# Kernel tuning notes

Hardware: AMD Instinct MI355X
Metric: run time of the kernel (lower is better)

The kernel has to match this reference:

```python
import jax, jax.numpy as jnp
import numpy as np

V = 30522
D = 768
K_DELTA = 768
BOTTLENECK = 512
B = 256
M = 4096
TEMP = 0.05
LAMBDA_REC = 1.0
LAMBDA_SPARSE = 1e-4
EPS = 1e-6


def setup_inputs() -> dict:
    key = jax.random.key(0)
    ks = jax.random.split(key, 10)
    s = lambda fan_in: 1.0 / np.sqrt(fan_in)
    return {
        "ht": jax.random.normal(ks[0], (B, V), jnp.float32),
        "sr": jax.random.uniform(ks[1], (B, V), jnp.float32),
        "z_pos": jax.random.normal(ks[2], (B, D), jnp.float32),
        "z_neg": jax.random.normal(ks[3], (M, D), jnp.float32),
        "zr": jax.random.normal(ks[4], (B, D), jnp.float32),
        "W1p": jax.random.normal(ks[5], (V, BOTTLENECK), jnp.float32) * s(V),
        "b1p": jnp.zeros((BOTTLENECK,), jnp.float32),
        "W2p": jax.random.normal(ks[6], (BOTTLENECK, V), jnp.float32) * s(BOTTLENECK),
        "b2p": jnp.zeros((V,), jnp.float32),
        "W1m": jax.random.normal(ks[7], (V, BOTTLENECK), jnp.float32) * s(V),
        "b1m": jnp.zeros((BOTTLENECK,), jnp.float32),
        "W2m": jax.random.normal(ks[8], (BOTTLENECK, V), jnp.float32) * s(BOTTLENECK),
        "b2m": jnp.zeros((V,), jnp.float32),
        "Wdec": jax.random.normal(ks[9], (V, D), jnp.float32) * s(V),
    }


def safe_l2norm(x, eps=EPS):
    return x / (jnp.linalg.norm(x, axis=-1, keepdims=True) + eps)


def _delta_branch(ht, W1, b1, W2, b2):
    # bottleneck MLP -> softplus -> topk -> scatter sparsify
    h = jax.nn.gelu(ht @ W1 + b1, approximate=False)  # torch nn.GELU default = exact erf
    u = jax.nn.softplus(h @ W2 + b2)                  # [B, V]
    vals, idx = jax.lax.top_k(u, K_DELTA)             # [B, K]
    rows = jnp.arange(u.shape[0])[:, None]
    return jnp.zeros_like(u).at[rows, idx].set(vals)  # sparse delta [B, V]


def reference(ht, sr, z_pos, z_neg, zr, W1p, b1p, W2p, b2p, W1m, b1m, W2m, b2m, Wdec):
    dsp = _delta_branch(ht, W1p, b1p, W2p, b2p)
    dsm = _delta_branch(ht, W1m, b1m, W2m, b2m)
    sqp = jnp.clip(sr + dsp, 0.0, None)
    sqm = jnp.clip(dsm, 0.0, None)
    sq = sqp - sqm
    zq = safe_l2norm(sq @ Wdec)        # DenseDecoder: Linear(V->D, bias=False) + l2norm
    zq = safe_l2norm(zq)               # re-normalized in forward_train
    z_pos_n = safe_l2norm(z_pos)
    z_neg_n = safe_l2norm(z_neg)

    pos_score = jnp.sum(zq * z_pos_n, axis=-1, keepdims=True)   # [B, 1]
    neg_score = zq @ z_neg_n.T                                   # [B, M]
    logits = jnp.concatenate([pos_score, neg_score], axis=1) / TEMP
    # cross entropy with label 0 for every row
    loss_retr = jnp.mean(jax.nn.logsumexp(logits, axis=-1) - logits[:, 0])

    zhat_r = safe_l2norm(sr @ Wdec)
    zr_n = safe_l2norm(zr)
    loss_rec = jnp.mean((zhat_r - zr_n) ** 2)

    loss_sparse = jnp.mean(jnp.sum(jnp.abs(dsp), axis=-1)) + jnp.mean(jnp.sum(jnp.abs(dsm), axis=-1))

    loss = loss_retr + LAMBDA_REC * loss_rec + LAMBDA_SPARSE * loss_sparse
    return loss
```

## Files before the change

### kernel.cpp

```cpp
#include <hip/hip_runtime.h>
#include <math.h>

#define VSZ   30522
#define DIM   768
#define KDELT 768
#define BOT   512
#define BATCH 256
#define MNEG  4096
#define EPSN  1e-6f
#define TEMPC 0.05f
#define INVT  20.0f
#define TKT   1024

typedef _Float16 f16;
typedef _Float16 f16x8 __attribute__((ext_vector_type(8)));
typedef _Float16 f16x2 __attribute__((ext_vector_type(2)));
typedef float    f32x4 __attribute__((ext_vector_type(4)));

static __device__ __forceinline__ float gelu_exact(float x){
    return 0.5f * x * (1.0f + erff(x * 0.70710678118654752440f));
}
static __device__ __forceinline__ float softplus_f(float x){
    return fmaxf(x, 0.0f) + log1pf(expf(-fabsf(x)));
}
static __device__ __forceinline__ f16x2 pkh(float a, float b){
    return __builtin_bit_cast(f16x2, __builtin_amdgcn_cvt_pkrtz(a, b));
}

template<int BSRC, int NG, int EPI, int LDA, int LDB, int N, int K, int NSPLIT>
__global__ __launch_bounds__(256, 3) void gemm32t(
    const float* __restrict__ A0, const float* __restrict__ A1,
    const float* __restrict__ B0, const float* __restrict__ B1,
    float* __restrict__ C0, float* __restrict__ C1,
    const float* __restrict__ bias0, const float* __restrict__ bias1)
{
    constexpr int MN = BATCH * N;
    __shared__ f16 Al[128][40];
    __shared__ f16 Bl[128][40];
    const int t  = threadIdx.x;
    const int m0 = blockIdx.x * 128;
    const int n0 = blockIdx.y * 128;
    const int br = blockIdx.z / NSPLIT;
    const int s  = blockIdx.z % NSPLIT;
    const float* __restrict__ A = br ? A1 : A0;
    const float* __restrict__ B = br ? B1 : B0;
    float* __restrict__ C       = br ? C1 : C0;
    const float* __restrict__ bias = br ? bias1 : bias0;

    constexpr int kchunk = ((K + NSPLIT * 32 - 1) / (NSPLIT * 32)) * 32;
    const int kb = s * kchunk;
    const int ke = min(K, kb + kchunk);

    const int ar4 = t >> 2;
    const int kq  = (t & 3) * 8;
    const int bn  = t & 127;
    const int bk2 = (t >> 7) * 16;

    const int lane = t & 63, w = t >> 6;
    const int wr = (w >> 1) * 64, wc = (w & 1) * 64;
    const int fr = lane & 15, kg = (lane >> 4) * 8;

    f32x4 acc[4][4] = {};

    float4 ra[2][2];
    float  rb[16];
    float4 rb2[2][2];

    union U8 { f16x8 v; f16x2 h[4]; };

    auto loadA = [&](int k0c, int krem) {
        #pragma unroll
        for (int p = 0; p < 2; p++) {
            const float* ap = A + (size_t)(m0 + p * 64 + ar4) * LDA + k0c + kq;
            if (krem == 32) {
                ra[p][0] = *(const float4*)ap;
                ra[p][1] = *(const float4*)(ap + 4);
            } else {
                float tm[8];
                #pragma unroll
                for (int i = 0; i < 8; i++) tm[i] = (kq + i < krem) ? ap[i] : 0.f;
                ra[p][0] = make_float4(tm[0], tm[1], tm[2], tm[3]);
                ra[p][1] = make_float4(tm[4], tm[5], tm[6], tm[7]);
            }
        }
    };
    auto loadB = [&](int k0c, int krem) {
        if (BSRC == 0) {
            const bool nok = (!NG) || (n0 + bn < N);
            if (krem == 32) {
                #pragma unroll
                for (int p = 0; p < 16; p++)
                    rb[p] = nok ? B[(size_t)(k0c + bk2 + p) * LDB + n0 + bn] : 0.f;
            } else {
                #pragma unroll
                for (int p = 0; p < 16; p++) {
                    const int kk = bk2 + p;
                    rb[p] = (kk < krem && nok) ? B[(size_t)(k0c + kk) * LDB + n0 + bn] : 0.f;
                }
            }
        } else {
            #pragma unroll
            for (int p = 0; p < 2; p++) {
                const float* bp = B + (size_t)(n0 + p * 64 + ar4) * LDB + k0c + kq;
                if (krem == 32) {
                    rb2[p][0] = *(const float4*)bp;
                    rb2[p][1] = *(const float4*)(bp + 4);
                } else {
                    float tm[8];
                    #pragma unroll
                    for (int i = 0; i < 8; i++) tm[i] = (kq + i < krem) ? bp[i] : 0.f;
                    rb2[p][0] = make_float4(tm[0], tm[1], tm[2], tm[3]);
                    rb2[p][1] = make_float4(tm[4], tm[5], tm[6], tm[7]);
                }
            }
        }
    };
    auto storeA = [&]() {
        #pragma unroll
        for (int p = 0; p < 2; p++) {
            U8 u;
            u.h[0] = pkh(ra[p][0].x, ra[p][0].y);
            u.h[1] = pkh(ra[p][0].z, ra[p][0].w);
            u.h[2] = pkh(ra[p][1].x, ra[p][1].y);
            u.h[3] = pkh(ra[p][1].z, ra[p][1].w);
            *(f16x8*)&Al[p * 64 + ar4][kq] = u.v;
        }
    };
    auto storeB = [&]() {
        if (BSRC == 0) {
            U8 u0, u1;
            u0.h[0] = pkh(rb[0],  rb[1]);
            u0.h[1] = pkh(rb[2],  rb[3]);
            u0.h[2] = pkh(rb[4],  rb[5]);
            u0.h[3] = pkh(rb[6],  rb[7]);
            u1.h[0] = pkh(rb[8],  rb[9]);
            u1.h[1] = pkh(rb[10], rb[11]);
            u1.h[2] = pkh(rb[12], rb[13]);
            u1.h[3] = pkh(rb[14], rb[15]);
            *(f16x8*)&Bl[bn][bk2]     = u0.v;
            *(f16x8*)&Bl[bn][bk2 + 8] = u1.v;
        } else {
            #pragma unroll
            for (int p = 0; p < 2; p++) {
                U8 u;
                u.h[0] = pkh(rb2[p][0].x, rb2[p][0].y);
                u.h[1] = pkh(rb2[p][0].z, rb2[p][0].w);
                u.h[2] = pkh(rb2[p][1].x, rb2[p][1].y);
                u.h[3] = pkh(rb2[p][1].z, rb2[p][1].w);
                *(f16x8*)&Bl[p * 64 + ar4][kq] = u.v;
            }
        }
    };

    int k0 = kb;
    {
        const int kr = min(32, ke - k0);
        loadA(k0, kr); loadB(k0, kr);
    }
    while (k0 < ke) {
        storeA(); storeB();
        __syncthreads();
        const int k1 = k0 + 32;
        if (k1 < ke) {
            const int kr = min(32, ke - k1);
            loadA(k1, kr); loadB(k1, kr);
        }
        f16x8 af[4], bf[4];
        #pragma unroll
        for (int m = 0; m < 4; m++) af[m] = *(const f16x8*)&Al[wr + m * 16 + fr][kg];
        #pragma unroll
        for (int n = 0; n < 4; n++) bf[n] = *(const f16x8*)&Bl[wc + n * 16 + fr][kg];
        #pragma unroll
        for (int m = 0; m < 4; m++)
            #pragma unroll
            for (int n = 0; n < 4; n++)
                acc[m][n] = __builtin_amdgcn_mfma_f32_16x16x32_f16(af[m], bf[n], acc[m][n], 0, 0, 0);
        __syncthreads();
        k0 = k1;
    }

    float* Cp = (EPI == 0) ? (C + (size_t)s * MN) : C;
    #pragma unroll
    for (int m = 0; m < 4; m++) {
        #pragma unroll
        for (int n = 0; n < 4; n++) {
            #pragma unroll
            for (int j = 0; j < 4; j++) {
                const int row = m0 + wr + m * 16 + (lane >> 4) * 4 + j;
                const int col = n0 + wc + n * 16 + fr;
                if (NG && col >= N) continue;
                if (EPI == 0) Cp[(size_t)row * N + col] = acc[m][n][j];
                else          Cp[(size_t)row * N + col] = softplus_f(acc[m][n][j] + bias[col]);
            }
        }
    }
}

__global__ __launch_bounds__(256) void reduce_bias_gelu2(
    const float* __restrict__ P0, const float* __restrict__ P1,
    const float* __restrict__ bias0, const float* __restrict__ bias1,
    float* __restrict__ H0, float* __restrict__ H1,
    int MN, int N, int nsplit)
{
    const int idx = blockIdx.x * 256 + threadIdx.x;
    if (idx >= MN) return;
    const int n = idx % N;
    const float* P = blockIdx.y ? P1 : P0;
    const float* bias = blockIdx.y ? bias1 : bias0;
    float* H = blockIdx.y ? H1 : H0;
    float s = 0.f;
    for (int k = 0; k < nsplit; k++) s += P[(size_t)k * MN + idx];
    H[idx] = gelu_exact(s + bias[n]);
}

__global__ __launch_bounds__(256) void reduce_sum_parts(
    const float* __restrict__ P, float* __restrict__ Y, int MN, int nsplit)
{
    const int idx = blockIdx.x * 256 + threadIdx.x;
    if (idx >= MN) return;
    float s = 0.f;
    for (int k = 0; k < nsplit; k++) s += P[(size_t)k * MN + idx];
    Y[idx] = s;
}

__global__ __launch_bounds__(TKT) void topk_thresh2(
    const float* __restrict__ U1, const float* __restrict__ U2,
    float* __restrict__ tP, float* __restrict__ tM)
{
    __shared__ unsigned int hist[4096];
    __shared__ unsigned int scan[TKT];
    __shared__ unsigned int s_pref;
    __shared__ int s_rem;
    const int row = blockIdx.y, t = threadIdx.x;
    const float* u = (blockIdx.x ? U2 : U1) + (size_t)row * VSZ;
    float* tout = blockIdx.x ? tM : tP;

    unsigned int pref = 0;
    int remain = KDELT;

    #pragma unroll
    for (int p = 0; p < 3; p++) {
        for (int i = t; i < 4096; i += TKT) hist[i] = 0;
        __syncthreads();
        for (int j = t; j < VSZ / 2; j += TKT) {
            const float2 x = *(const float2*)(u + 2 * j);
            const unsigned int v0 = __float_as_uint(x.x);
            const unsigned int v1 = __float_as_uint(x.y);
            if (p == 0) {
                atomicAdd(&hist[v0 >> 19], 1u);
                atomicAdd(&hist[v1 >> 19], 1u);
            } else if (p == 1) {
                if ((v0 >> 19) == pref) atomicAdd(&hist[(v0 >> 7) & 0xFFFu], 1u);
                if ((v1 >> 19) == pref) atomicAdd(&hist[(v1 >> 7) & 0xFFFu], 1u);
            } else {
                if ((v0 >> 7) == pref) atomicAdd(&hist[v0 & 0x7Fu], 1u);
                if ((v1 >> 7) == pref) atomicAdd(&hist[v1 & 0x7Fu], 1u);
            }
        }
        __syncthreads();
        unsigned int loc = hist[4 * t] + hist[4 * t + 1] + hist[4 * t + 2] + hist[4 * t + 3];
        scan[t] = loc;
        __syncthreads();
        for (int o = 1; o < TKT; o <<= 1) {
            const unsigned int v = (t + o < TKT) ? scan[t + o] : 0u;
            __syncthreads();
            scan[t] += v;
            __syncthreads();
        }
        const unsigned int above = (t + 1 < TKT) ? scan[t + 1] : 0u;
        if (scan[t] >= (unsigned int)remain && above < (unsigned int)remain) {
            unsigned int cum = above;
            #pragma unroll
            for (int bi = 3; bi >= 0; bi--) {
                const int b = 4 * t + bi;
                cum += hist[b];
                if (cum >= (unsigned int)remain) {
                    s_pref = (unsigned int)b;
                    s_rem  = remain - (int)(cum - hist[b]);
                    break;
                }
            }
        }
        __syncthreads();
        if (p == 0)      pref = s_pref;
        else if (p == 1) pref = (pref << 12) | s_pref;
        else             pref = (pref << 7)  | s_pref;
        remain = s_rem;
        __syncthreads();
    }
    if (t == 0) tout[row] = __uint_as_float(pref);
}

__global__ __launch_bounds__(256) void build_sq(
    float* __restrict__ U1, const float* __restrict__ U2,
    const float* __restrict__ sr,
    const float* __restrict__ tp, const float* __restrict__ tm,
    float* __restrict__ sparse_p, float* __restrict__ sparse_m)
{
    __shared__ float red[256];
    const int row = blockIdx.x, t = threadIdx.x;
    const float thp = tp[row], thm = tm[row];
    float* u1 = U1 + (size_t)row * VSZ;
    const float* u2 = U2 + (size_t)row * VSZ;
    const float* s  = sr + (size_t)row * VSZ;
    float sp = 0.f, sm = 0.f;
    for (int j = t; j < VSZ / 2; j += 256) {
        const float2 up = *(const float2*)(u1 + 2 * j);
        const float2 um = *(const float2*)(u2 + 2 * j);
        const float2 ss = *(const float2*)(s  + 2 * j);
        const float dp0 = (up.x >= thp) ? up.x : 0.f;
        const float dp1 = (up.y >= thp) ? up.y : 0.f;
        const float dm0 = (um.x >= thm) ? um.x : 0.f;
        const float dm1 = (um.y >= thm) ? um.y : 0.f;
        sp += dp0 + dp1; sm += dm0 + dm1;
        float2 o;
        o.x = fmaxf(ss.x + dp0, 0.f) - fmaxf(dm0, 0.f);
        o.y = fmaxf(ss.y + dp1, 0.f) - fmaxf(dm1, 0.f);
        *(float2*)(u1 + 2 * j) = o;
    }
    red[t] = sp; __syncthreads();
    for (int o = 128; o > 0; o >>= 1) { if (t < o) red[t] += red[t + o]; __syncthreads(); }
    if (t == 0) sparse_p[row] = red[0];
    __syncthreads();
    red[t] = sm; __syncthreads();
    for (int o = 128; o > 0; o >>= 1) { if (t < o) red[t] += red[t + o]; __syncthreads(); }
    if (t == 0) sparse_m[row] = red[0];
}

__global__ __launch_bounds__(256) void rownorm(
    const float* __restrict__ X, float* __restrict__ Y, int dbl)
{
    __shared__ float red[256];
    const int row = blockIdx.x, t = threadIdx.x;
    const float* x = X + (size_t)row * DIM;
    float* y = Y + (size_t)row * DIM;
    float v0 = x[t], v1 = x[t + 256], v2 = x[t + 512];
    red[t] = v0 * v0 + v1 * v1 + v2 * v2; __syncthreads();
    for (int o = 128; o > 0; o >>= 1) { if (t < o) red[t] += red[t + o]; __syncthreads(); }
    const float nrm = sqrtf(red[0]) + EPSN;
    v0 /= nrm; v1 /= nrm; v2 /= nrm;
    if (dbl) {
        __syncthreads();
        red[t] = v0 * v0 + v1 * v1 + v2 * v2; __syncthreads();
        for (int o = 128; o > 0; o >>= 1) { if (t < o) red[t] += red[t + o]; __syncthreads(); }
        const float n2 = sqrtf(red[0]) + EPSN;
        v0 /= n2; v1 /= n2; v2 /= n2;
    }
    y[t] = v0; y[t + 256] = v1; y[t + 512] = v2;
}

__global__ __launch_bounds__(256) void pos_dot(
    const float* __restrict__ zq, const float* __restrict__ zp,
    float* __restrict__ posL)
{
    __shared__ float red[256];
    const int row = blockIdx.x, t = threadIdx.x;
    const float* a = zq + (size_t)row * DIM;
    const float* b = zp + (size_t)row * DIM;
    red[t] = a[t] * b[t] + a[t + 256] * b[t + 256] + a[t + 512] * b[t + 512];
    __syncthreads();
    for (int o = 128; o > 0; o >>= 1) { if (t < o) red[t] += red[t + o]; __syncthreads(); }
    if (t == 0) posL[row] = red[0] / TEMPC;
}

__global__ __launch_bounds__(256) void lse_loss(
    const float* __restrict__ negL, const float* __restrict__ posL,
    float* __restrict__ rowL)
{
    __shared__ float red[256];
    const int row = blockIdx.x, t = threadIdx.x;
    const float* nl = negL + (size_t)row * MNEG;
    const float p = posL[row];
    float lmax = (t == 0) ? p : -INFINITY;
    for (int j = t; j < MNEG; j += 256) lmax = fmaxf(lmax, nl[j] * INVT);
    red[t] = lmax; __syncthreads();
    for (int o = 128; o > 0; o >>= 1) { if (t < o) red[t] = fmaxf(red[t], red[t + o]); __syncthreads(); }
    const float mx = red[0];
    __syncthreads();
    float lsum = (t == 0) ? expf(p - mx) : 0.f;
    for (int j = t; j < MNEG; j += 256) lsum += expf(nl[j] * INVT - mx);
    red[t] = lsum; __syncthreads();
    for (int o = 128; o > 0; o >>= 1) { if (t < o) red[t] += red[t + o]; __syncthreads(); }
    if (t == 0) rowL[row] = mx + logf(red[0]) - p;
}

__global__ __launch_bounds__(256) void rec_row(
    const float* __restrict__ zhat, const float* __restrict__ zrn,
    float* __restrict__ part)
{
    __shared__ float red[256];
    const int row = blockIdx.x, t = threadIdx.x;
    const float* a = zhat + (size_t)row * DIM;
    const float* b = zrn + (size_t)row * DIM;
    const float d0 = a[t] - b[t], d1 = a[t + 256] - b[t + 256], d2 = a[t + 512] - b[t + 512];
    red[t] = d0 * d0 + d1 * d1 + d2 * d2;
    __syncthreads();
    for (int o = 128; o > 0; o >>= 1) { if (t < o) red[t] += red[t + o]; __syncthreads(); }
    if (t == 0) part[row] = red[0];
}

__global__ __launch_bounds__(256) void final_combine(
    const float* __restrict__ rowL, const float* __restrict__ recP,
    const float* __restrict__ spP, const float* __restrict__ spM,
    float* __restrict__ out)
{
    __shared__ float red[256];
    const int t = threadIdx.x;
    red[t] = rowL[t]; __syncthreads();
    for (int o = 128; o > 0; o >>= 1) { if (t < o) red[t] += red[t + o]; __syncthreads(); }
    const float retr = red[0] / 256.0f;
    __syncthreads();
    red[t] = recP[t]; __syncthreads();
    for (int o = 128; o > 0; o >>= 1) { if (t < o) red[t] += red[t + o]; __syncthreads(); }
    const float rec = red[0] / (float)(BATCH * DIM);
    __syncthreads();
    red[t] = spP[t] + spM[t]; __syncthreads();
    for (int o = 128; o > 0; o >>= 1) { if (t < o) red[t] += red[t + o]; __syncthreads(); }
    const float sparse = red[0] / 256.0f;
    if (t == 0) out[0] = retr + 1.0f * rec + 1e-4f * sparse;
}

extern "C" void kernel_launch(void* const* d_in, const int* in_sizes, int n_in,
                              void* d_out, int out_size, void* d_ws, size_t ws_size,
                              hipStream_t stream)
{
    const float* ht   = (const float*)d_in[0];
    const float* sr   = (const float*)d_in[1];
    const float* zpos = (const float*)d_in[2];
    const float* zneg = (const float*)d_in[3];
    const float* zr   = (const float*)d_in[4];
    const float* W1p  = (const float*)d_in[5];
    const float* b1p  = (const float*)d_in[6];
    const float* W2p  = (const float*)d_in[7];
    const float* b2p  = (const float*)d_in[8];
    const float* W1m  = (const float*)d_in[9];
    const float* b1m  = (const float*)d_in[10];
    const float* W2m  = (const float*)d_in[11];
    const float* b2m  = (const float*)d_in[12];
    const float* Wdec = (const float*)d_in[13];
    float* out = (float*)d_out;

    char* ws = (char*)d_ws;
    float* U1   = (float*)(ws + 0);
    float* U2   = (float*)(ws + 31254528);
    float* P    = (float*)(ws + 62509056);
    float* Hp   = (float*)(ws + 96063488);
    float* Hm   = (float*)(ws + 96587776);
    float* Y1   = (float*)(ws + 97112064);
    float* Y2   = (float*)(ws + 97898496);
    float* Zn   = (float*)(ws + 98684928);
    float* Zp   = (float*)(ws + 111267840);
    float* Zrn  = (float*)(ws + 112054272);
    float* NegL = (float*)(ws + 112840704);
    float* tP   = (float*)(ws + 117035008);
    float* tM   = tP + 256;
    float* spP  = tP + 512;
    float* spM  = tP + 768;
    float* posL = tP + 1024;
    float* rowL = tP + 1280;
    float* recP = tP + 1536;
    (void)in_sizes; (void)n_in; (void)out_size; (void)ws_size;

    const dim3 blk(256);

    gemm32t<0,0,0, VSZ, BOT, BOT, VSZ, 56><<<dim3(2,4,112), blk, 0, stream>>>(
        ht, ht, W1p, W1m, U1, U2, nullptr, nullptr);
    reduce_bias_gelu2<<<dim3(512,2), blk, 0, stream>>>(
        U1, U2, b1p, b1m, Hp, Hm, BATCH*BOT, BOT, 56);

    gemm32t<0,1,1, BOT, VSZ, VSZ, BOT, 1><<<dim3(2,239,2), blk, 0, stream>>>(
        Hp, Hm, W2p, W2m, U1, U2, b2p, b2m);

    topk_thresh2<<<dim3(2,256), dim3(TKT), 0, stream>>>(U1, U2, tP, tM);
    build_sq<<<dim3(256), blk, 0, stream>>>(U1, U2, sr, tP, tM, spP, spM);

    gemm32t<0,0,0, VSZ, DIM, DIM, VSZ, 32><<<dim3(2,6,64), blk, 0, stream>>>(
        U1, sr, Wdec, Wdec, P, U2, nullptr, nullptr);
    reduce_sum_parts<<<dim3(768), blk, 0, stream>>>(P,  Y1, BATCH*DIM, 32);
    reduce_sum_parts<<<dim3(768), blk, 0, stream>>>(U2, Y2, BATCH*DIM, 32);

    rownorm<<<dim3(256),  blk, 0, stream>>>(Y1, Y1, 1);
    rownorm<<<dim3(256),  blk, 0, stream>>>(Y2, Y2, 0);
    rownorm<<<dim3(4096), blk, 0, stream>>>(zneg, Zn, 0);
    rownorm<<<dim3(256),  blk, 0, stream>>>(zpos, Zp, 0);
    rownorm<<<dim3(256),  blk, 0, stream>>>(zr,   Zrn, 0);

    pos_dot<<<dim3(256), blk, 0, stream>>>(Y1, Zp, posL);
    gemm32t<1,0,0, DIM, DIM, MNEG, DIM, 8><<<dim3(2,32,8), blk, 0, stream>>>(
        Y1, Y1, Zn, Zn, P, P, nullptr, nullptr);
    reduce_sum_parts<<<dim3(4096), blk, 0, stream>>>(P, NegL, BATCH*MNEG, 8);
    lse_loss<<<dim3(256), blk, 0, stream>>>(NegL, posL, rowL);

    rec_row<<<dim3(256), blk, 0, stream>>>(Y2, Zrn, recP);

    final_combine<<<dim3(1), blk, 0, stream>>>(rowL, recP, spP, spM, out);
}
```

Measured before the change: 466.6 us.

## Double-buffer LDS and prefetch registers in split-K GEMM, reduce split counts

The GEMM main loop now uses two LDS buffers and two register staging sets, so global loads for tile k+2 are issued while tile k is computed, and one barrier per iteration is removed. Launch bounds drop from 3 to 2 blocks per CU because LDS and register use grow. The first GEMM's split-K drops from 56 to 32 and writes partials into the P workspace. The negatives GEMM split drops from 8 to 4, which means fewer partial sums to reduce but fewer blocks to run in parallel.

```diff
diff --git a/kernel.cpp b/kernel.cpp
--- a/kernel.cpp
+++ b/kernel.cpp
@@ -28,15 +28,17 @@
 }
 
 template<int BSRC, int NG, int EPI, int LDA, int LDB, int N, int K, int NSPLIT>
-__global__ __launch_bounds__(256, 3) void gemm32t(
+__global__ __launch_bounds__(256, 2) void gemm32t(
     const float* __restrict__ A0, const float* __restrict__ A1,
     const float* __restrict__ B0, const float* __restrict__ B1,
     float* __restrict__ C0, float* __restrict__ C1,
     const float* __restrict__ bias0, const float* __restrict__ bias1)
 {
     constexpr int MN = BATCH * N;
-    __shared__ f16 Al[128][40];
-    __shared__ f16 Bl[128][40];
+    __shared__ f16 Al0[128][40];
+    __shared__ f16 Bl0[128][40];
+    __shared__ f16 Al1[128][40];
+    __shared__ f16 Bl1[128][40];
     const int t  = threadIdx.x;
     const int m0 = blockIdx.x * 128;
     const int n0 = blockIdx.y * 128;
@@ -62,13 +64,13 @@
 
     f32x4 acc[4][4] = {};
 
-    float4 ra[2][2];
-    float  rb[16];
-    float4 rb2[2][2];
+    float4 raS0[2][2], raS1[2][2];
+    float  rbS0[16],   rbS1[16];
+    float4 rb2S0[2][2], rb2S1[2][2];
 
     union U8 { f16x8 v; f16x2 h[4]; };
 
-    auto loadA = [&](int k0c, int krem) {
+    auto loadA = [&](int k0c, int krem, float4 (&ra)[2][2]) {
         #pragma unroll
         for (int p = 0; p < 2; p++) {
             const float* ap = A + (size_t)(m0 + p * 64 + ar4) * LDA + k0c + kq;
@@ -84,7 +86,7 @@
             }
         }
     };
-    auto loadB = [&](int k0c, int krem) {
+    auto loadB = [&](int k0c, int krem, float (&rb)[16], float4 (&rb2)[2][2]) {
         if (BSRC == 0) {
             const bool nok = (!NG) || (n0 + bn < N);
             if (krem == 32) {
@@ -115,7 +117,7 @@
             }
         }
     };
-    auto storeA = [&]() {
+    auto storeA = [&](float4 (&ra)[2][2], f16 (&Al)[128][40]) {
         #pragma unroll
         for (int p = 0; p < 2; p++) {
             U8 u;
@@ -126,7 +128,7 @@
             *(f16x8*)&Al[p * 64 + ar4][kq] = u.v;
         }
     };
-    auto storeB = [&]() {
+    auto storeB = [&](float (&rb)[16], float4 (&rb2)[2][2], f16 (&Bl)[128][40]) {
         if (BSRC == 0) {
             U8 u0, u1;
             u0.h[0] = pkh(rb[0],  rb[1]);
@@ -151,20 +153,7 @@
             }
         }
     };
-
-    int k0 = kb;
-    {
-        const int kr = min(32, ke - k0);
-        loadA(k0, kr); loadB(k0, kr);
-    }
-    while (k0 < ke) {
-        storeA(); storeB();
-        __syncthreads();
-        const int k1 = k0 + 32;
-        if (k1 < ke) {
-            const int kr = min(32, ke - k1);
-            loadA(k1, kr); loadB(k1, kr);
-        }
+    auto compute = [&](f16 (&Al)[128][40], f16 (&Bl)[128][40]) {
         f16x8 af[4], bf[4];
         #pragma unroll
         for (int m = 0; m < 4; m++) af[m] = *(const f16x8*)&Al[wr + m * 16 + fr][kg];
@@ -175,8 +164,43 @@
             #pragma unroll
             for (int n = 0; n < 4; n++)
                 acc[m][n] = __builtin_amdgcn_mfma_f32_16x16x32_f16(af[m], bf[n], acc[m][n], 0, 0, 0);
-        __syncthreads();
-        k0 = k1;
+    };
+
+    int k_next = kb;
+    {
+        const int kr = min(32, ke - k_next);
+        loadA(k_next, kr, raS0); loadB(k_next, kr, rbS0, rb2S0);
+        k_next += 32;
+    }
+    if (k_next < ke) {
+        const int kr = min(32, ke - k_next);
+        loadA(k_next, kr, raS1); loadB(k_next, kr, rbS1, rb2S1);
+        k_next += 32;
+    }
+
+    int k_comp = kb;
+    while (true) {
+        storeA(raS0, Al0); storeB(rbS0, rb2S0, Bl0);
+        if (k_next < ke) {
+            const int kr = min(32, ke - k_next);
+            loadA(k_next, kr, raS0); loadB(k_next, kr, rbS0, rb2S0);
+            k_next += 32;
+        }
+        __syncthreads();
+        compute(Al0, Bl0);
+        k_comp += 32;
+        if (k_comp >= ke) break;
+
+        storeA(raS1, Al1); storeB(rbS1, rb2S1, Bl1);
+        if (k_next < ke) {
+            const int kr = min(32, ke - k_next);
+            loadA(k_next, kr, raS1); loadB(k_next, kr, rbS1, rb2S1);
+            k_next += 32;
+        }
+        __syncthreads();
+        compute(Al1, Bl1);
+        k_comp += 32;
+        if (k_comp >= ke) break;
     }
 
     float* Cp = (EPI == 0) ? (C + (size_t)s * MN) : C;
@@ -444,6 +468,7 @@
     float* U1   = (float*)(ws + 0);
     float* U2   = (float*)(ws + 31254528);
     float* P    = (float*)(ws + 62509056);
+    float* P1g  = (float*)(ws + 62509056 + 16777216);
     float* Hp   = (float*)(ws + 96063488);
     float* Hm   = (float*)(ws + 96587776);
     float* Y1   = (float*)(ws + 97112064);
@@ -463,10 +488,10 @@
 
     const dim3 blk(256);
 
-    gemm32t<0,0,0, VSZ, BOT, BOT, VSZ, 56><<<dim3(2,4,112), blk, 0, stream>>>(
-        ht, ht, W1p, W1m, U1, U2, nullptr, nullptr);
+    gemm32t<0,0,0, VSZ, BOT, BOT, VSZ, 32><<<dim3(2,4,64), blk, 0, stream>>>(
+        ht, ht, W1p, W1m, P, P1g, nullptr, nullptr);
     reduce_bias_gelu2<<<dim3(512,2), blk, 0, stream>>>(
-        U1, U2, b1p, b1m, Hp, Hm, BATCH*BOT, BOT, 56);
+        P, P1g, b1p, b1m, Hp, Hm, BATCH*BOT, BOT, 32);
 
     gemm32t<0,1,1, BOT, VSZ, VSZ, BOT, 1><<<dim3(2,239,2), blk, 0, stream>>>(
         Hp, Hm, W2p, W2m, U1, U2, b2p, b2m);
@@ -486,9 +511,9 @@
     rownorm<<<dim3(256),  blk, 0, stream>>>(zr,   Zrn, 0);
 
     pos_dot<<<dim3(256), blk, 0, stream>>>(Y1, Zp, posL);
-    gemm32t<1,0,0, DIM, DIM, MNEG, DIM, 8><<<dim3(2,32,8), blk, 0, stream>>>(
+    gemm32t<1,0,0, DIM, DIM, MNEG, DIM, 4><<<dim3(2,32,4), blk, 0, stream>>>(
         Y1, Y1, Zn, Zn, P, P, nullptr, nullptr);
-    reduce_sum_parts<<<dim3(4096), blk, 0, stream>>>(P, NegL, BATCH*MNEG, 8);
+    reduce_sum_parts<<<dim3(4096), blk, 0, stream>>>(P, NegL, BATCH*MNEG, 4);
     lse_loss<<<dim3(256), blk, 0, stream>>>(NegL, posL, rowL);
 
     rec_row<<<dim3(256), blk, 0, stream>>>(Y2, Zrn, recP);
```

After: 509.5 us. +9.2%, slower.
